# Kernel optimization log

Hardware: AMD Instinct MI355X
Metric: run time of the kernel (lower is better)

The kernel has to match this reference:

```python
import jax, jax.numpy as jnp
import numpy as np

K = 3
EPS = 1e-5

def diff_conv(x, Tf, Tb, W, b):
    terms = [x]
    xf = x
    for _ in range(K):
        xf = jnp.einsum('mn,bnc->bmc', Tf, xf)
        terms.append(xf)
    xb = x
    for _ in range(K):
        xb = jnp.einsum('mn,bnc->bmc', Tb, xb)
        terms.append(xb)
    z = jnp.concatenate(terms, axis=-1)  # (B,N,(2K+1)*C)
    return z @ W + b

def layer_norm(x, gamma, beta):
    mu = jnp.mean(x, axis=-1, keepdims=True)
    var = jnp.var(x, axis=-1, keepdims=True)
    return (x - mu) * jax.lax.rsqrt(var + EPS) * gamma + beta

def dcgru_cell(x, h, Tf, Tb, Wg, bg, Wc, bc, gamma, beta):
    xh = jnp.concatenate([x, h], axis=-1)
    gates = jax.nn.sigmoid(diff_conv(xh, Tf, Tb, Wg, bg))
    r, u = jnp.split(gates, 2, axis=-1)
    xrh = jnp.concatenate([x, r * h], axis=-1)
    c = jnp.tanh(diff_conv(xrh, Tf, Tb, Wc, bc))
    h_new = (1.0 - u) * h + u * c
    return layer_norm(h_new, gamma, beta)

def setup_inputs() -> dict:
    key = jax.random.key(0)
    B, T, N, F, H = 32, 8, 512, 16, 128
    ks = jax.random.split(key, 16)
    s = 0.02
    n_terms = 2 * K + 1
    d0 = (F + H) * n_terms   # layer 0 combined diffusion dim
    d1 = (H + H) * n_terms   # layer 1
    inp = {
        'x_seq': jax.random.normal(ks[0], (B, T, N, F), dtype=jnp.float32),
        'T_f': jax.random.uniform(ks[1], (N, N), dtype=jnp.float32) / N,
        'T_b': jax.random.uniform(ks[2], (N, N), dtype=jnp.float32) / N,
        'Wg0': jax.random.normal(ks[3], (d0, 2 * H), dtype=jnp.float32) * s,
        'bg0': jnp.zeros((2 * H,), dtype=jnp.float32),
        'Wc0': jax.random.normal(ks[4], (d0, H), dtype=jnp.float32) * s,
        'bc0': jnp.zeros((H,), dtype=jnp.float32),
        'g0': jnp.ones((H,), dtype=jnp.float32),
        'be0': jnp.zeros((H,), dtype=jnp.float32),
        'Wg1': jax.random.normal(ks[5], (d1, 2 * H), dtype=jnp.float32) * s,
        'bg1': jnp.zeros((2 * H,), dtype=jnp.float32),
        'Wc1': jax.random.normal(ks[6], (d1, H), dtype=jnp.float32) * s,
        'bc1': jnp.zeros((H,), dtype=jnp.float32),
        'g1': jnp.ones((H,), dtype=jnp.float32),
        'be1': jnp.zeros((H,), dtype=jnp.float32),
    }
    return inp

def reference(x_seq, T_f, T_b, Wg0, bg0, Wc0, bc0, g0, be0, Wg1, bg1, Wc1, bc1, g1, be1):
    B, T, N, F = x_seq.shape
    H = g0.shape[0]
    h0 = jnp.zeros((B, N, H), dtype=x_seq.dtype)
    h1 = jnp.zeros((B, N, H), dtype=x_seq.dtype)

    def step(carry, x_t):
        h0, h1 = carry
        h0 = dcgru_cell(x_t, h0, T_f, T_b, Wg0, bg0, Wc0, bc0, g0, be0)
        h1 = dcgru_cell(h0, h1, T_f, T_b, Wg1, bg1, Wc1, bc1, g1, be1)
        return (h0, h1), None

    xs = jnp.swapaxes(x_seq, 0, 1)  # (T,B,N,F)
    (h0, h1), _ = jax.lax.scan(step, (h0, h1), xs)
    return (h0, h1)
```

## Files before the change

### kernel.cpp

```cpp
#include <hip/hip_runtime.h>
#include <hip/hip_bf16.h>
#include <math.h>

typedef unsigned short u16;
typedef __attribute__((ext_vector_type(8))) short short8;
typedef __attribute__((ext_vector_type(4))) float f32x4;

__device__ __forceinline__ u16 f2bf(float f) {
  union { float f; unsigned u; } v; v.f = f;
  unsigned r = v.u + 0x7fffu + ((v.u >> 16) & 1u);
  return (u16)(r >> 16);
}

__device__ __forceinline__ void glds16(const u16* g, u16* l) {
  __builtin_amdgcn_global_load_lds(
      (const __attribute__((address_space(1))) void*)g,
      (__attribute__((address_space(3))) void*)l, 16, 0, 0);
}

template<int N> __device__ __forceinline__ void kbar() {
  asm volatile("s_waitcnt vmcnt(%0)" :: "n"(N) : "memory");
  __builtin_amdgcn_s_barrier();
  asm volatile("" ::: "memory");
}
__device__ __forceinline__ void bar2() {
  asm volatile("" ::: "memory");
  __builtin_amdgcn_s_barrier();
  asm volatile("" ::: "memory");
}

template<int BM, int BN, int WR, int WC>
__global__ __launch_bounds__(256) void gemm_diff(
    const u16* __restrict__ Tpow, const u16* __restrict__ zT,
    u16* __restrict__ zout, int ldz, int C, int coff0,
    u16* __restrict__ zdual, int Fdual)
{
  constexpr int BK = 64;
  constexpr int FM = BM / (WR * 16), FN = BN / (WC * 16);
  constexpr int SLOTS = (BM + BN) * 8;
  constexpr int NS = (SLOTS + 255) / 256;
  constexpr int VMIN = SLOTS / 256;
  constexpr int HALF = (BM + BN) * BK;
  __shared__ u16 sm[2 * HALF];
  const int tid = threadIdx.x, lane = tid & 63, wid = tid >> 6;
  const int wr = wid / WC, wc = wid % WC;
  const int l15 = lane & 15, l4 = lane >> 4;
  const int m0 = blockIdx.x * BM;
  const int y0 = blockIdx.y * BN;
  const int b = blockIdx.z / 6, tc = blockIdx.z % 6;
  const u16* A = Tpow + (long)tc * 262144;
  const u16* Bz = zT + (long)y0 * 16384 + b * 512;
  const int lb = (tid - lane) * 8;

  const u16* gp[NS];
  #pragma unroll
  for (int i = 0; i < NS; i++) {
    int s = tid + i * 256;
    int row = s >> 3, kc = s & 7;
    int kcg = kc ^ (row & 7);
    gp[i] = (row < BM) ? A + (long)(m0 + row) * 512 + kcg * 8
                       : Bz + (long)(row - BM) * 16384 + kcg * 8;
  }

  auto stage = [&](int buf) {
    u16* base = sm + buf * HALF + lb;
    #pragma unroll
    for (int i = 0; i < NS; i++) {
      if (i * 256 + 256 <= SLOTS || tid < SLOTS - i * 256)
        glds16(gp[i], base + i * 2048);
    }
    #pragma unroll
    for (int i = 0; i < NS; i++) gp[i] += BK;
  };

  f32x4 acc[FM][FN] = {};
  auto compute = [&](int buf) {
    const u16* smc = sm + buf * HALF;
    #pragma unroll
    for (int kk = 0; kk < 2; kk++) {
      short8 af[FM], bf[FN];
      #pragma unroll
      for (int i = 0; i < FM; i++) {
        int ar = wr * FM * 16 + i * 16 + l15;
        af[i] = *(const short8*)&smc[ar * BK + (((kk * 4 + l4) ^ (ar & 7)) << 3)];
      }
      #pragma unroll
      for (int j = 0; j < FN; j++) {
        int br = wc * FN * 16 + j * 16 + l15;
        bf[j] = *(const short8*)&smc[BM * BK + br * BK + (((kk * 4 + l4) ^ (br & 7)) << 3)];
      }
      #pragma unroll
      for (int i = 0; i < FM; i++)
        #pragma unroll
        for (int j = 0; j < FN; j++)
          acc[i][j] = __builtin_amdgcn_mfma_f32_16x16x32_bf16(af[i], bf[j], acc[i][j], 0, 0, 0);
    }
  };

  stage(0);
  int cur = 0;
  for (int t = 0; t < 7; t++) {
    stage(cur ^ 1);
    kbar<VMIN>();
    compute(cur);
    bar2();
    cur ^= 1;
  }
  kbar<0>();
  compute(cur);

  const int tC = (1 + tc) * C;
  #pragma unroll
  for (int i = 0; i < FM; i++) {
    #pragma unroll
    for (int j = 0; j < FN; j++) {
      int node = m0 + wr * FM * 16 + i * 16 + l4 * 4;
      int ch = y0 + wc * FN * 16 + j * 16 + l15;
      #pragma unroll
      for (int rr = 0; rr < 4; rr++) {
        u16 v = f2bf(acc[i][j][rr]);
        long r = (long)b * 512 + node + rr;
        zout[r * ldz + tC + coff0 + ch] = v;
        if (Fdual && ch < Fdual) zdual[r * ldz + tC + ch] = v;
      }
    }
  }
}

template<int BM, int BN>
__global__ __launch_bounds__(256) void gemm_proj(
    const u16* __restrict__ Az, int ldA,
    const u16* __restrict__ W, int K,
    const float* __restrict__ bias,
    const float* __restrict__ hst,
    u16* __restrict__ zc, int ldzc, int Foff,
    u16* __restrict__ zTc,
    float* __restrict__ outbuf)
{
  constexpr int BK = 64;
  constexpr int FM = BM / 32, FN = BN / 32;
  constexpr int NSA = BM / 32, NSB = BN / 32;
  constexpr int VMIN = NSA + NSB;
  constexpr int HALF = (BM + BN) * BK;
  __shared__ u16 sm[2 * HALF];
  const int tid = threadIdx.x, lane = tid & 63, wid = tid >> 6;
  const int wr = wid >> 1, wc = wid & 1;
  const int l15 = lane & 15, l4 = lane >> 4;
  const int m0 = blockIdx.x * BM;
  const int n0 = blockIdx.y * BN;
  const int lb = (tid - lane) * 8;

  const u16* ap[NSA];
  const u16* wp[NSB];
  #pragma unroll
  for (int i = 0; i < NSA; i++) {
    int s = tid + i * 256;
    int row = s >> 3, kc = s & 7;
    int kcg = kc ^ (row & 7);
    ap[i] = Az + (long)(m0 + row) * ldA + kcg * 8;
  }
  #pragma unroll
  for (int i = 0; i < NSB; i++) {
    int s = tid + (NSA + i) * 256;
    int row = s >> 3, kc = s & 7;
    int kcg = kc ^ (row & 7);
    wp[i] = W + (long)(n0 + row - BM) * K + kcg * 8;
  }

  auto stage = [&](int buf) {
    u16* base = sm + buf * HALF + lb;
    #pragma unroll
    for (int i = 0; i < NSA; i++) { glds16(ap[i], base + i * 2048); ap[i] += BK; }
    #pragma unroll
    for (int i = 0; i < NSB; i++) { glds16(wp[i], base + (NSA + i) * 2048); wp[i] += BK; }
  };

  f32x4 acc[FM][FN] = {};
  auto compute = [&](int buf) {
    const u16* smc = sm + buf * HALF;
    #pragma unroll
    for (int kk = 0; kk < 2; kk++) {
      short8 af[FM], bf[FN];
      #pragma unroll
      for (int i = 0; i < FM; i++) {
        int ar = wr * FM * 16 + i * 16 + l15;
        af[i] = *(const short8*)&smc[ar * BK + (((kk * 4 + l4) ^ (ar & 7)) << 3)];
      }
      #pragma unroll
      for (int j = 0; j < FN; j++) {
        int br = wc * FN * 16 + j * 16 + l15;
        bf[j] = *(const short8*)&smc[BM * BK + br * BK + (((kk * 4 + l4) ^ (br & 7)) << 3)];
      }
      #pragma unroll
      for (int i = 0; i < FM; i++)
        #pragma unroll
        for (int j = 0; j < FN; j++)
          acc[i][j] = __builtin_amdgcn_mfma_f32_16x16x32_bf16(af[i], bf[j], acc[i][j], 0, 0, 0);
    }
  };

  stage(0);
  int cur = 0;
  const int NT = K >> 6;
  for (int t = 1; t < NT; t++) {
    stage(cur ^ 1);
    kbar<VMIN>();
    compute(cur);
    bar2();
    cur ^= 1;
  }
  kbar<0>();
  compute(cur);

  #pragma unroll
  for (int i = 0; i < FM; i++) {
    #pragma unroll
    for (int j = 0; j < FN; j++) {
      int mb = m0 + wr * FM * 16 + i * 16 + l4 * 4;
      int n = n0 + wc * FN * 16 + j * 16 + l15;
      #pragma unroll
      for (int rr = 0; rr < 4; rr++) {
        float v = acc[i][j][rr] + bias[n];
        long r = mb + rr;
        float g = 1.f / (1.f + expf(-v));
        if (n < 128) {
          float rh = g * hst[r * 128 + n];
          u16 hv = f2bf(rh);
          zc[r * ldzc + Foff + n] = hv;
          zTc[(long)n * 16384 + r] = hv;
        } else {
          outbuf[r * 128 + (n - 128)] = g;
        }
      }
    }
  }
}

__global__ __launch_bounds__(256) void proj_cand_gru(
    const u16* __restrict__ Ag, const u16* __restrict__ Ac, int ldA,
    const u16* __restrict__ W, int K,
    const float* __restrict__ bias,
    const float* __restrict__ ub, float* __restrict__ h,
    const float* __restrict__ gamma, const float* __restrict__ beta,
    u16* __restrict__ rm0, int ld0, int co0,
    u16* __restrict__ rm1, int ld1, int co1,
    u16* __restrict__ cm0, int ro0,
    u16* __restrict__ cm1, int ro1,
    const float* __restrict__ xs, int tnext,
    u16* __restrict__ xz0g, u16* __restrict__ xz0c, u16* __restrict__ xz0T)
{
  constexpr int BM = 32, BN = 128, BK = 64;
  constexpr int FM = 2, FN = 2;
  constexpr int NSA = 1, NSB = 4;
  constexpr int HALF = (BM + BN) * BK;
  __shared__ u16 sm[2 * HALF];
  const int tid = threadIdx.x, lane = tid & 63, wid = tid >> 6;
  const int wc = wid;
  const int l15 = lane & 15, l4 = lane >> 4;
  const int m0 = blockIdx.x * BM;
  const int lb = (tid - lane) * 8;

  unsigned aoff[NSA];
  const u16* wp[NSB];
  #pragma unroll
  for (int i = 0; i < NSA; i++) {
    int s = tid + i * 256;
    int row = s >> 3, kc = s & 7;
    int kcg = kc ^ (row & 7);
    aoff[i] = (unsigned)((m0 + row) * ldA + kcg * 8);
  }
  #pragma unroll
  for (int i = 0; i < NSB; i++) {
    int s = tid + (NSA + i) * 256;
    int row = (s >> 3) - BM, kc = s & 7;
    int kcg = kc ^ ((row + BM) & 7);
    wp[i] = W + (long)row * K + kcg * 8;
  }

  auto stage = [&](int buf, int koff) {
    u16* base = sm + buf * HALF + lb;
    const u16* ab = ((koff >> 7) & 1) ? Ac : Ag;
    #pragma unroll
    for (int i = 0; i < NSA; i++) glds16(ab + aoff[i] + koff, base + i * 2048);
    #pragma unroll
    for (int i = 0; i < NSB; i++) { glds16(wp[i], base + (NSA + i) * 2048); wp[i] += BK; }
  };

  f32x4 acc[FM][FN] = {};
  auto compute = [&](int buf) {
    const u16* smc = sm + buf * HALF;
    #pragma unroll
    for (int kk = 0; kk < 2; kk++) {
      short8 af[FM], bf[FN];
      #pragma unroll
      for (int i = 0; i < FM; i++) {
        int ar = i * 16 + l15;
        af[i] = *(const short8*)&smc[ar * BK + (((kk * 4 + l4) ^ (ar & 7)) << 3)];
      }
      #pragma unroll
      for (int j = 0; j < FN; j++) {
        int br = wc * 32 + j * 16 + l15;
        bf[j] = *(const short8*)&smc[BM * BK + br * BK + (((kk * 4 + l4) ^ (br & 7)) << 3)];
      }
      #pragma unroll
      for (int i = 0; i < FM; i++)
        #pragma unroll
        for (int j = 0; j < FN; j++)
          acc[i][j] = __builtin_amdgcn_mfma_f32_16x16x32_bf16(af[i], bf[j], acc[i][j], 0, 0, 0);
    }
  };

  stage(0, 0);
  int cur = 0;
  const int NT = K >> 6;
  for (int t = 1; t < NT; t++) {
    stage(cur ^ 1, t * 64);
    kbar<5>();
    compute(cur);
    bar2();
    cur ^= 1;
  }
  kbar<0>();
  compute(cur);
  __syncthreads();

  float* hs = (float*)sm;
  #pragma unroll
  for (int i = 0; i < FM; i++) {
    #pragma unroll
    for (int j = 0; j < FN; j++) {
      #pragma unroll
      for (int rr = 0; rr < 4; rr++) {
        int lrow = i * 16 + l4 * 4 + rr;
        int n = wc * 32 + j * 16 + l15;
        long r = m0 + lrow;
        float c = tanhf(acc[i][j][rr] + bias[n]);
        float u = ub[r * 128 + n];
        float hold = h[r * 128 + n];
        hs[lrow * 132 + n] = (1.f - u) * hold + u * c;
      }
    }
  }
  __syncthreads();

  {
    int row = tid >> 3, g = tid & 7;
    float s = 0.f, s2 = 0.f;
    #pragma unroll
    for (int k = 0; k < 16; k++) {
      float v = hs[row * 132 + g + 8 * k];
      s += v; s2 += v * v;
    }
    s += __shfl_xor(s, 1); s2 += __shfl_xor(s2, 1);
    s += __shfl_xor(s, 2); s2 += __shfl_xor(s2, 2);
    s += __shfl_xor(s, 4); s2 += __shfl_xor(s2, 4);
    float mu = s * (1.f / 128.f);
    float var = s2 * (1.f / 128.f) - mu * mu;
    float rs = rsqrtf(var + 1e-5f);
    long rb = (long)(m0 + row) * 128;
    #pragma unroll
    for (int k = 0; k < 16; k++) {
      int c = g + 8 * k;
      float v = (hs[row * 132 + c] - mu) * rs * gamma[c] + beta[c];
      h[rb + c] = v;
      hs[row * 132 + c] = v;
    }
  }
  __syncthreads();

  #pragma unroll
  for (int i = 0; i < 16; i++) {
    int idx = tid + i * 256;
    int row = idx >> 7, c = idx & 127;
    u16 v = f2bf(hs[row * 132 + c]);
    long r = m0 + row;
    rm0[r * ld0 + co0 + c] = v;
    if (rm1) rm1[r * ld1 + co1 + c] = v;
  }
  {
    const int c2 = tid >> 1, half = tid & 1;
    u16 tmp[16];
    #pragma unroll
    for (int i = 0; i < 16; i++) tmp[i] = f2bf(hs[(half * 16 + i) * 132 + c2]);
    const short8* tv = (const short8*)tmp;
    long off = (long)(ro0 + c2) * 16384 + m0 + half * 16;
    *(short8*)&cm0[off] = tv[0];
    *(short8*)&cm0[off + 8] = tv[1];
    if (cm1) {
      long o2 = (long)(ro1 + c2) * 16384 + m0 + half * 16;
      *(short8*)&cm1[o2] = tv[0];
      *(short8*)&cm1[o2 + 8] = tv[1];
    }
  }
  if (xs) {
    for (int e = tid; e < 512; e += 256) {
      int lrow = e >> 4, f = e & 15;
      long r = m0 + lrow;
      int b = (int)(r >> 9), n = (int)(r & 511);
      u16 v = f2bf(xs[(((long)b * 8 + tnext) * 512 + n) * 16 + f]);
      xz0g[r * 1024 + f] = v;
      xz0c[r * 1024 + f] = v;
      xz0T[(long)f * 16384 + r] = v;
    }
  }
}

__global__ __launch_bounds__(256) void xk(
    const float* __restrict__ xs, int t,
    u16* __restrict__ z0g, u16* __restrict__ z0c, u16* __restrict__ z0Tg)
{
  int r = blockIdx.x * 256 + threadIdx.x;
  int b = r >> 9, n = r & 511;
  const float* src = xs + (((long)b * 8 + t) * 512 + n) * 16;
  u16 tmp[16];
  #pragma unroll
  for (int f = 0; f < 16; f++) tmp[f] = f2bf(src[f]);
  const short8* tv = (const short8*)tmp;
  *(short8*)&z0g[(long)r * 1024] = tv[0];
  *(short8*)&z0g[(long)r * 1024 + 8] = tv[1];
  *(short8*)&z0c[(long)r * 1024] = tv[0];
  *(short8*)&z0c[(long)r * 1024 + 8] = tv[1];
  #pragma unroll
  for (int f = 0; f < 16; f++) z0Tg[(long)f * 16384 + r] = tmp[f];
}

__global__ void zero_cols(u16* __restrict__ z, int ld, int c0) {
  int idx = blockIdx.x * 256 + threadIdx.x;
  int r = idx >> 4, s = idx & 15;
  short8 zz = {};
  *(short8*)&z[(long)r * ld + c0 + s * 8] = zz;
}

__global__ void cvtT(const float* __restrict__ Tf, const float* __restrict__ Tb,
                     u16* __restrict__ Tpow, u16* __restrict__ TfT, u16* __restrict__ TbT)
{
  int idx = blockIdx.x * 256 + threadIdx.x;
  int i = idx >> 9, j = idx & 511;
  const float* s = blockIdx.y ? Tb : Tf;
  u16* d = Tpow + (blockIdx.y ? 3 : 0) * 262144;
  u16* dT = blockIdx.y ? TbT : TfT;
  u16 v = f2bf(s[idx]);
  d[idx] = v;
  dT[(long)j * 512 + i] = v;
}

__global__ __launch_bounds__(256) void gemm_pow(
    const u16* __restrict__ A0, const u16* __restrict__ B0, u16* __restrict__ C0,
    const u16* __restrict__ A1, const u16* __restrict__ B1, u16* __restrict__ C1)
{
  constexpr int BM = 64, BN = 64, BK = 32;
  __shared__ u16 sm[(BM + BN) * BK];
  const int tid = threadIdx.x, lane = tid & 63, wid = tid >> 6;
  const int wr = wid >> 1, wc = wid & 1;
  const int l15 = lane & 15, l4 = lane >> 4;
  const int m0 = blockIdx.x * BM, n0 = blockIdx.y * BN;
  const u16* A = blockIdx.z ? A1 : A0;
  const u16* Bt = blockIdx.z ? B1 : B0;
  u16* Cc = blockIdx.z ? C1 : C0;

  f32x4 acc[2][2] = {};
  for (int k0 = 0; k0 < 512; k0 += BK) {
    for (int s = tid; s < (BM + BN) * 4; s += 256) {
      const u16* gp;
      if (s < BM * 4) { int m = s >> 2, kc = s & 3; gp = A + (long)(m0 + m) * 512 + k0 + kc * 8; }
      else { int q = s - BM * 4; int n = q >> 2, kc = q & 3; gp = Bt + (long)(n0 + n) * 512 + k0 + kc * 8; }
      glds16(gp, sm + (s - lane) * 8);
    }
    __syncthreads();
    short8 af[2], bf[2];
    #pragma unroll
    for (int i = 0; i < 2; i++)
      af[i] = *(const short8*)&sm[(wr * 32 + i * 16 + l15) * BK + l4 * 8];
    #pragma unroll
    for (int j = 0; j < 2; j++)
      bf[j] = *(const short8*)&sm[BM * BK + (wc * 32 + j * 16 + l15) * BK + l4 * 8];
    #pragma unroll
    for (int i = 0; i < 2; i++)
      #pragma unroll
      for (int j = 0; j < 2; j++)
        acc[i][j] = __builtin_amdgcn_mfma_f32_16x16x32_bf16(af[i], bf[j], acc[i][j], 0, 0, 0);
    __syncthreads();
  }
  #pragma unroll
  for (int i = 0; i < 2; i++)
    #pragma unroll
    for (int j = 0; j < 2; j++) {
      int mb = m0 + wr * 32 + i * 16 + l4 * 4;
      int n = n0 + wc * 32 + j * 16 + l15;
      #pragma unroll
      for (int rr = 0; rr < 4; rr++)
        Cc[(long)(mb + rr) * 512 + n] = f2bf(acc[i][j][rr]);
    }
}

__global__ void wt_cvt(const float* __restrict__ W, u16* __restrict__ Wt,
                       int Ksrc, int Kpad, int Nout) {
  long idx = (long)blockIdx.x * 256 + threadIdx.x;
  if (idx >= (long)Nout * Kpad) return;
  int o = (int)(idx / Kpad), k = (int)(idx % Kpad);
  Wt[idx] = f2bf(k < Ksrc ? W[(long)k * Nout + o] : 0.f);
}

extern "C" void kernel_launch(void* const* d_in, const int* in_sizes, int n_in,
                              void* d_out, int out_size, void* d_ws, size_t ws_size,
                              hipStream_t stream) {
  const float* x_seq = (const float*)d_in[0];
  const float* Tf  = (const float*)d_in[1];
  const float* Tb  = (const float*)d_in[2];
  const float* Wg0 = (const float*)d_in[3];
  const float* bg0 = (const float*)d_in[4];
  const float* Wc0 = (const float*)d_in[5];
  const float* bc0 = (const float*)d_in[6];
  const float* g0  = (const float*)d_in[7];
  const float* be0 = (const float*)d_in[8];
  const float* Wg1 = (const float*)d_in[9];
  const float* bg1 = (const float*)d_in[10];
  const float* Wc1 = (const float*)d_in[11];
  const float* bc1 = (const float*)d_in[12];
  const float* g1  = (const float*)d_in[13];
  const float* be1 = (const float*)d_in[14];

  constexpr int B = 32, T = 8;
  constexpr long M = 16384;

  char* p = (char*)d_ws;
  auto carve = [&](size_t bytes) { char* r = p; p += (bytes + 255) & ~(size_t)255; return r; };
  u16* z0g  = (u16*)carve(M * 1024 * 2);
  u16* z0c  = (u16*)carve(M * 1024 * 2);
  u16* z1g  = (u16*)carve(M * 1792 * 2);
  u16* z1c  = (u16*)carve(M * 1792 * 2);
  u16* z0Tg = (u16*)carve(144L * M * 2);
  u16* z0Tc = (u16*)carve(128L * M * 2);
  u16* z1Tg = (u16*)carve(256L * M * 2);
  u16* z1Tc = (u16*)carve(128L * M * 2);
  float* ubuf = (float*)carve(M * 128 * 4);
  u16* Tpow = (u16*)carve(6L * 512 * 512 * 2);
  u16* TfT  = (u16*)carve(512L * 512 * 2);
  u16* TbT  = (u16*)carve(512L * 512 * 2);
  u16* Wg0t = (u16*)carve(256L * 1024 * 2);
  u16* Wc0t = (u16*)carve(128L * 1024 * 2);
  u16* Wg1t = (u16*)carve(256L * 1792 * 2);
  u16* Wc1t = (u16*)carve(128L * 1792 * 2);

  float* h0 = (float*)d_out;
  float* h1 = h0 + M * 128;

  hipMemsetAsync(d_out, 0, (size_t)out_size * 4, stream);
  zero_cols<<<1024, 256, 0, stream>>>(z0g, 1024, 16);
  zero_cols<<<1024, 256, 0, stream>>>(z1g, 1792, 128);
  hipMemsetAsync(z0Tg + 16L * M, 0, 128L * M * 2, stream);
  hipMemsetAsync(z1Tg + 128L * M, 0, 128L * M * 2, stream);

  cvtT<<<dim3(1024, 2), 256, 0, stream>>>(Tf, Tb, Tpow, TfT, TbT);
  gemm_pow<<<dim3(8, 8, 2), 256, 0, stream>>>(
      Tpow, TfT, Tpow + 1L * 262144, Tpow + 3L * 262144, TbT, Tpow + 4L * 262144);
  gemm_pow<<<dim3(8, 8, 2), 256, 0, stream>>>(
      Tpow + 1L * 262144, TfT, Tpow + 2L * 262144, Tpow + 4L * 262144, TbT, Tpow + 5L * 262144);
  wt_cvt<<<(256 * 1024 + 255) / 256, 256, 0, stream>>>(Wg0, Wg0t, 1008, 1024, 256);
  wt_cvt<<<(128 * 1024 + 255) / 256, 256, 0, stream>>>(Wc0, Wc0t, 1008, 1024, 128);
  wt_cvt<<<(256 * 1792 + 255) / 256, 256, 0, stream>>>(Wg1, Wg1t, 1792, 1792, 256);
  wt_cvt<<<(128 * 1792 + 255) / 256, 256, 0, stream>>>(Wc1, Wc1t, 1792, 1792, 128);

  xk<<<64, 256, 0, stream>>>(x_seq, 0, z0g, z0c, z0Tg);

  for (int t = 0; t < T; t++) {
    gemm_diff<128, 48, 4, 1><<<dim3(4, 3, 6 * B), 256, 0, stream>>>(
        Tpow, z0Tg, z0g, 1024, 144, 0, z0c, 16);
    gemm_proj<64, 64><<<dim3(256, 4), 256, 0, stream>>>(
        z0g, 1024, Wg0t, 1024, bg0, h0, z0c, 1024, 16, z0Tc, ubuf);
    gemm_diff<128, 64, 2, 2><<<dim3(4, 2, 6 * B), 256, 0, stream>>>(
        Tpow, z0Tc, z0c, 1024, 144, 16, nullptr, 0);
    proj_cand_gru<<<512, 256, 0, stream>>>(
        z0c, z0c, 1024, Wc0t, 1024, bc0, ubuf, h0, g0, be0,
        z0g, 1024, 16, z1g, 1792, 0, z0Tg, 16, z1Tg, 0,
        nullptr, 0, nullptr, nullptr, nullptr);
    gemm_diff<128, 64, 2, 2><<<dim3(4, 4, 6 * B), 256, 0, stream>>>(
        Tpow, z1Tg, z1g, 1792, 256, 0, nullptr, 0);
    gemm_proj<64, 64><<<dim3(256, 4), 256, 0, stream>>>(
        z1g, 1792, Wg1t, 1792, bg1, h1, z1c, 1792, 128, z1Tc, ubuf);
    gemm_diff<128, 64, 2, 2><<<dim3(4, 2, 6 * B), 256, 0, stream>>>(
        Tpow, z1Tc, z1c, 1792, 256, 128, nullptr, 0);
    proj_cand_gru<<<512, 256, 0, stream>>>(
        z1g, z1c, 1792, Wc1t, 1792, bc1, ubuf, h1, g1, be1,
        z1g, 1792, 128, nullptr, 0, 0, z1Tg, 128, nullptr, 0,
        (t < T - 1) ? x_seq : nullptr, t + 1, z0g, z0c, z0Tg);
  }
}
```

Before: 1.583 ms.

## Process two batches per diffusion GEMM block and skip zero-state work at t=0

Each gemm_diff block now loads one tile of the diffusion-power matrix and multiplies it against two batch slices, halving A-tile reloads and the number of blocks along z (96 instead of 192). Launch bounds request two blocks per CU to bound register use. At the first timestep the hidden state is zero, so diffusion over the hidden-state columns is skipped or narrowed, relying on the buffers being zero-filled by a single large memset. This adds LDS and register pressure per block and ties correctness to the zero-initialization of the z buffers.

```diff
diff --git a/kernel.cpp b/kernel.cpp
--- a/kernel.cpp
+++ b/kernel.cpp
@@ -30,36 +30,39 @@
 }
 
 template<int BM, int BN, int WR, int WC>
-__global__ __launch_bounds__(256) void gemm_diff(
+__global__ __launch_bounds__(256, 2) void gemm_diff(
     const u16* __restrict__ Tpow, const u16* __restrict__ zT,
     u16* __restrict__ zout, int ldz, int C, int coff0,
     u16* __restrict__ zdual, int Fdual)
 {
   constexpr int BK = 64;
   constexpr int FM = BM / (WR * 16), FN = BN / (WC * 16);
-  constexpr int SLOTS = (BM + BN) * 8;
+  constexpr int SLOTS = (BM + 2 * BN) * 8;
   constexpr int NS = (SLOTS + 255) / 256;
   constexpr int VMIN = SLOTS / 256;
-  constexpr int HALF = (BM + BN) * BK;
+  constexpr int HALF = (BM + 2 * BN) * BK;
   __shared__ u16 sm[2 * HALF];
   const int tid = threadIdx.x, lane = tid & 63, wid = tid >> 6;
   const int wr = wid / WC, wc = wid % WC;
   const int l15 = lane & 15, l4 = lane >> 4;
   const int m0 = blockIdx.x * BM;
   const int y0 = blockIdx.y * BN;
-  const int b = blockIdx.z / 6, tc = blockIdx.z % 6;
+  const int b0 = (blockIdx.z / 6) * 2, tc = blockIdx.z % 6;
   const u16* A = Tpow + (long)tc * 262144;
-  const u16* Bz = zT + (long)y0 * 16384 + b * 512;
   const int lb = (tid - lane) * 8;
 
   const u16* gp[NS];
   #pragma unroll
   for (int i = 0; i < NS; i++) {
     int s = tid + i * 256;
-    int row = s >> 3, kc = s & 7;
-    int kcg = kc ^ (row & 7);
-    gp[i] = (row < BM) ? A + (long)(m0 + row) * 512 + kcg * 8
-                       : Bz + (long)(row - BM) * 16384 + kcg * 8;
+    if (s < BM * 8) {
+      int row = s >> 3, kc = s & 7;
+      gp[i] = A + (long)(m0 + row) * 512 + (kc ^ (row & 7)) * 8;
+    } else {
+      int s2 = s - BM * 8;
+      int q = s2 / (BN * 8), n = (s2 % (BN * 8)) >> 3, kc = s2 & 7;
+      gp[i] = zT + (long)(y0 + n) * 16384 + (b0 + q) * 512 + (kc ^ (n & 7)) * 8;
+    }
   }
 
   auto stage = [&](int buf) {
@@ -73,27 +76,32 @@
     for (int i = 0; i < NS; i++) gp[i] += BK;
   };
 
-  f32x4 acc[FM][FN] = {};
+  f32x4 acc[2][FM][FN] = {};
   auto compute = [&](int buf) {
     const u16* smc = sm + buf * HALF;
     #pragma unroll
     for (int kk = 0; kk < 2; kk++) {
-      short8 af[FM], bf[FN];
+      short8 af[FM], bf[2][FN];
       #pragma unroll
       for (int i = 0; i < FM; i++) {
         int ar = wr * FM * 16 + i * 16 + l15;
         af[i] = *(const short8*)&smc[ar * BK + (((kk * 4 + l4) ^ (ar & 7)) << 3)];
       }
       #pragma unroll
-      for (int j = 0; j < FN; j++) {
-        int br = wc * FN * 16 + j * 16 + l15;
-        bf[j] = *(const short8*)&smc[BM * BK + br * BK + (((kk * 4 + l4) ^ (br & 7)) << 3)];
-      }
-      #pragma unroll
-      for (int i = 0; i < FM; i++)
+      for (int q = 0; q < 2; q++)
         #pragma unroll
-        for (int j = 0; j < FN; j++)
-          acc[i][j] = __builtin_amdgcn_mfma_f32_16x16x32_bf16(af[i], bf[j], acc[i][j], 0, 0, 0);
+        for (int j = 0; j < FN; j++) {
+          int br = wc * FN * 16 + j * 16 + l15;
+          bf[q][j] = *(const short8*)&smc[BM * BK + q * BN * BK + br * BK +
+                                          (((kk * 4 + l4) ^ (br & 7)) << 3)];
+        }
+      #pragma unroll
+      for (int q = 0; q < 2; q++)
+        #pragma unroll
+        for (int i = 0; i < FM; i++)
+          #pragma unroll
+          for (int j = 0; j < FN; j++)
+            acc[q][i][j] = __builtin_amdgcn_mfma_f32_16x16x32_bf16(af[i], bf[q][j], acc[q][i][j], 0, 0, 0);
     }
   };
 
@@ -111,17 +119,20 @@
 
   const int tC = (1 + tc) * C;
   #pragma unroll
-  for (int i = 0; i < FM; i++) {
-    #pragma unroll
-    for (int j = 0; j < FN; j++) {
-      int node = m0 + wr * FM * 16 + i * 16 + l4 * 4;
-      int ch = y0 + wc * FN * 16 + j * 16 + l15;
-      #pragma unroll
-      for (int rr = 0; rr < 4; rr++) {
-        u16 v = f2bf(acc[i][j][rr]);
-        long r = (long)b * 512 + node + rr;
-        zout[r * ldz + tC + coff0 + ch] = v;
-        if (Fdual && ch < Fdual) zdual[r * ldz + tC + ch] = v;
+  for (int q = 0; q < 2; q++) {
+    #pragma unroll
+    for (int i = 0; i < FM; i++) {
+      #pragma unroll
+      for (int j = 0; j < FN; j++) {
+        int node = m0 + wr * FM * 16 + i * 16 + l4 * 4;
+        int ch = y0 + wc * FN * 16 + j * 16 + l15;
+        #pragma unroll
+        for (int rr = 0; rr < 4; rr++) {
+          u16 v = f2bf(acc[q][i][j][rr]);
+          long r = (long)(b0 + q) * 512 + node + rr;
+          zout[r * ldz + tC + coff0 + ch] = v;
+          if (Fdual && ch < Fdual) zdual[r * ldz + tC + ch] = v;
+        }
       }
     }
   }
@@ -424,13 +435,6 @@
   for (int f = 0; f < 16; f++) z0Tg[(long)f * 16384 + r] = tmp[f];
 }
 
-__global__ void zero_cols(u16* __restrict__ z, int ld, int c0) {
-  int idx = blockIdx.x * 256 + threadIdx.x;
-  int r = idx >> 4, s = idx & 15;
-  short8 zz = {};
-  *(short8*)&z[(long)r * ld + c0 + s * 8] = zz;
-}
-
 __global__ void cvtT(const float* __restrict__ Tf, const float* __restrict__ Tb,
                      u16* __restrict__ Tpow, u16* __restrict__ TfT, u16* __restrict__ TbT)
 {
@@ -546,8 +550,7 @@
   float* h1 = h0 + M * 128;
 
   hipMemsetAsync(d_out, 0, (size_t)out_size * 4, stream);
-  zero_cols<<<1024, 256, 0, stream>>>(z0g, 1024, 16);
-  zero_cols<<<1024, 256, 0, stream>>>(z1g, 1792, 128);
+  hipMemsetAsync(z0g, 0, (size_t)((char*)(z1c + M * 1792) - (char*)z0g), stream);
   hipMemsetAsync(z0Tg + 16L * M, 0, 128L * M * 2, stream);
   hipMemsetAsync(z1Tg + 128L * M, 0, 128L * M * 2, stream);
 
@@ -564,22 +567,29 @@
   xk<<<64, 256, 0, stream>>>(x_seq, 0, z0g, z0c, z0Tg);
 
   for (int t = 0; t < T; t++) {
-    gemm_diff<128, 48, 4, 1><<<dim3(4, 3, 6 * B), 256, 0, stream>>>(
-        Tpow, z0Tg, z0g, 1024, 144, 0, z0c, 16);
+    if (t == 0) {
+      gemm_diff<128, 16, 4, 1><<<dim3(4, 1, 96), 256, 0, stream>>>(
+          Tpow, z0Tg, z0g, 1024, 144, 0, z0c, 16);
+    } else {
+      gemm_diff<128, 48, 4, 1><<<dim3(4, 3, 96), 256, 0, stream>>>(
+          Tpow, z0Tg, z0g, 1024, 144, 0, z0c, 16);
+    }
     gemm_proj<64, 64><<<dim3(256, 4), 256, 0, stream>>>(
         z0g, 1024, Wg0t, 1024, bg0, h0, z0c, 1024, 16, z0Tc, ubuf);
-    gemm_diff<128, 64, 2, 2><<<dim3(4, 2, 6 * B), 256, 0, stream>>>(
-        Tpow, z0Tc, z0c, 1024, 144, 16, nullptr, 0);
+    if (t > 0)
+      gemm_diff<128, 64, 2, 2><<<dim3(4, 2, 96), 256, 0, stream>>>(
+          Tpow, z0Tc, z0c, 1024, 144, 16, nullptr, 0);
     proj_cand_gru<<<512, 256, 0, stream>>>(
         z0c, z0c, 1024, Wc0t, 1024, bc0, ubuf, h0, g0, be0,
         z0g, 1024, 16, z1g, 1792, 0, z0Tg, 16, z1Tg, 0,
         nullptr, 0, nullptr, nullptr, nullptr);
-    gemm_diff<128, 64, 2, 2><<<dim3(4, 4, 6 * B), 256, 0, stream>>>(
+    gemm_diff<128, 64, 2, 2><<<dim3(4, (t == 0) ? 2 : 4, 96), 256, 0, stream>>>(
         Tpow, z1Tg, z1g, 1792, 256, 0, nullptr, 0);
     gemm_proj<64, 64><<<dim3(256, 4), 256, 0, stream>>>(
         z1g, 1792, Wg1t, 1792, bg1, h1, z1c, 1792, 128, z1Tc, ubuf);
-    gemm_diff<128, 64, 2, 2><<<dim3(4, 2, 6 * B), 256, 0, stream>>>(
-        Tpow, z1Tc, z1c, 1792, 256, 128, nullptr, 0);
+    if (t > 0)
+      gemm_diff<128, 64, 2, 2><<<dim3(4, 2, 96), 256, 0, stream>>>(
+          Tpow, z1Tc, z1c, 1792, 256, 128, nullptr, 0);
     proj_cand_gru<<<512, 256, 0, stream>>>(
         z1g, z1c, 1792, Wc1t, 1792, bc1, ubuf, h1, g1, be1,
         z1g, 1792, 128, nullptr, 0, 0, z1Tg, 128, nullptr, 0,
```

Result: faster. 1.486 ms (-6.1%).
